# Kernel optimization log

Measured on AMD Instinct MI355X. Metric: run time of the kernel, lower is better.

Reference implementation:

```python
import jax, jax.numpy as jnp
import numpy as np

TOKENS, IN_DIM, VOCAB = 2048, 2048, 32000
TILE_FACTOR = 16


def setup_inputs() -> dict:
    key = jax.random.key(0)
    k1, k2, k3 = jax.random.split(key, 3)
    inp = jax.random.normal(k1, (TOKENS, IN_DIM), dtype=jnp.float32)
    target = jax.random.randint(k2, (TOKENS,), 0, VOCAB, dtype=jnp.int64)
    # LM-head weight, shape [out_dim(vocab), in_dim] as in nn.Linear
    proj_weight = jax.random.normal(k3, (VOCAB, IN_DIM), dtype=jnp.float32) * 0.02
    return {"input": inp, "target": target, "proj_weight": proj_weight}


def reference(input, target, proj_weight):
    # Original loops over token tiles: for each tile, logits = tile @ W.T,
    # then softmax over vocab (dim=-1). Softmax is per-row (per-token), so the
    # concatenation of per-tile outputs equals the full row-wise softmax.
    # target is accepted but unused, matching the original forward.
    logits = jnp.einsum('td,vd->tv', input, proj_weight)  # [tokens, vocab]
    return jax.nn.softmax(logits, axis=-1)
```

## Files before the change

kernel.cpp:

```cpp
#include <hip/hip_runtime.h>
#include <hip/hip_bf16.h>
#include <math.h>

#define TOKENS 2048
#define IN_DIM 2048
#define VOCAB  32000

#define BM 256
#define BN 256
#define BK 64
#define NKSTEP (IN_DIM / BK)
#define GEMM_GRID ((TOKENS / BM) * (VOCAB / BN))
#define NCT (VOCAB / BN)

typedef short s16x8 __attribute__((ext_vector_type(8)));
typedef float f32x4 __attribute__((ext_vector_type(4)));

__device__ __forceinline__ unsigned short f2bf_rne(float f) {
  unsigned int u = __float_as_uint(f);
  u += 0x7fffu + ((u >> 16) & 1u);
  return (unsigned short)(u >> 16);
}
__device__ __forceinline__ float bf2f(unsigned short h) {
  return __uint_as_float(((unsigned int)h) << 16);
}

__global__ __launch_bounds__(256) void convert_all(
    const float* __restrict__ x, const float* __restrict__ w,
    unsigned short* __restrict__ xbf, unsigned short* __restrict__ wbf) {
  const int NX = TOKENS * IN_DIM / 4;
  const int NW = VOCAB * IN_DIM / 4;
  int idx = blockIdx.x * blockDim.x + threadIdx.x;
  int stride = gridDim.x * blockDim.x;
  for (int i = idx; i < NX + NW; i += stride) {
    const bool isx = i < NX;
    const int j = isx ? i : i - NX;
    float4 v = isx ? reinterpret_cast<const float4*>(x)[j]
                   : reinterpret_cast<const float4*>(w)[j];
    ushort4 o;
    o.x = f2bf_rne(v.x);
    o.y = f2bf_rne(v.y);
    o.z = f2bf_rne(v.z);
    o.w = f2bf_rne(v.w);
    if (isx)
      reinterpret_cast<ushort4*>(xbf)[j] = o;
    else
      reinterpret_cast<ushort4*>(wbf)[j] = o;
  }
}

__device__ __forceinline__ void gload_lds16(const unsigned short* g, unsigned short* l) {
  __builtin_amdgcn_global_load_lds(
      (const __attribute__((address_space(1))) unsigned int*)g,
      (__attribute__((address_space(3))) unsigned int*)l, 16, 0, 0);
}

__global__ __launch_bounds__(512, 2) void gemm_bt(
    const unsigned short* __restrict__ A,
    const unsigned short* __restrict__ B,
    unsigned short* __restrict__ CB,
    float2* __restrict__ partials) {
  __shared__ __align__(16) unsigned short lds[65536];

  const int tid = threadIdx.x;
  const int lane = tid & 63;
  const int wave = tid >> 6;
  const int wr = wave >> 2;
  const int wc = wave & 3;

  const int bid = blockIdx.x;
  const int lid = (bid & 7) * (GEMM_GRID / 8) + (bid >> 3);
  const int rowTile = lid & 7;
  const int colTile = lid >> 3;
  const int rowBase = rowTile * BM;
  const int colBase = colTile * BN;

  const int r0 = tid >> 3;
  const int r1 = 64 + r0;
  const int c8 = (((tid & 7) ^ (r0 & 7)) << 3);
  const unsigned short* srcA0 = A + (size_t)(rowBase + r0) * IN_DIM + c8;
  const unsigned short* srcA1 = A + (size_t)(rowBase + r1) * IN_DIM + c8;
  const unsigned short* srcB0 = B + (size_t)(colBase + r0) * IN_DIM + c8;
  const unsigned short* srcB1 = B + (size_t)(colBase + r1) * IN_DIM + c8;
  const int ldsD0 = tid * 8;
  const int ldsD1 = (512 + tid) * 8;

  auto stageA = [&](int buf, int h, int k) {
    size_t off = (size_t)h * (128 * IN_DIM) + k;
    int dst = buf * 32768 + h * 8192;
    gload_lds16(srcA0 + off, &lds[dst + ldsD0]);
    gload_lds16(srcA1 + off, &lds[dst + ldsD1]);
  };
  auto stageB = [&](int buf, int h, int k) {
    size_t off = (size_t)h * (128 * IN_DIM) + k;
    int dst = 16384 + buf * 32768 + h * 8192;
    gload_lds16(srcB0 + off, &lds[dst + ldsD0]);
    gload_lds16(srcB1 + off, &lds[dst + ldsD1]);
  };

  const int sc0 = (((lane >> 4) ^ (lane & 7)) << 3);
  const int sc1 = (((4 + (lane >> 4)) ^ (lane & 7)) << 3);
  const int aRow = (wr * 128 + (lane & 15)) * 64;
  const int bRow = 16384 + (wc * 64 + (lane & 15)) * 64;

#define LDA(buf, m, kk) (*(const s16x8*)&lds[(buf) * 32768 + aRow + (m) * 1024 + ((kk) ? sc1 : sc0)])
#define LDB(buf, n, kk) (*(const s16x8*)&lds[(buf) * 32768 + bRow + (n) * 1024 + ((kk) ? sc1 : sc0)])

  f32x4 acc[8][4] = {};

  stageA(0, 0, 0);
  stageA(0, 1, 0);
  stageB(0, 0, 0);
  stageB(0, 1, 0);
  stageA(1, 0, 64);
  stageA(1, 1, 64);
  stageB(1, 0, 64);
  asm volatile("s_waitcnt vmcnt(6)" ::: "memory");
  __builtin_amdgcn_s_barrier();

#define KSTEP(bufc, kn1, kn2)                                                       \
  {                                                                                 \
    s16x8 aL[4][2], aH[4][2], bL[2][2], bH[2][2];                                   \
                                   \
    _Pragma("unroll") for (int m = 0; m < 4; ++m) {                                 \
      aL[m][0] = LDA(bufc, m, 0);                                                   \
      aL[m][1] = LDA(bufc, m, 1);                                                   \
    }                                                                               \
    _Pragma("unroll") for (int n = 0; n < 2; ++n) {                                 \
      bL[n][0] = LDB(bufc, n, 0);                                                   \
      bL[n][1] = LDB(bufc, n, 1);                                                   \
    }                                                                               \
    stageB((bufc) ^ 1, 1, kn1);                                                     \
    asm volatile("s_waitcnt lgkmcnt(8)" ::: "memory");                              \
    __builtin_amdgcn_s_barrier();                                                   \
    asm volatile("s_waitcnt lgkmcnt(0)" ::: "memory");                              \
    __builtin_amdgcn_s_setprio(1);                                                  \
    _Pragma("unroll") for (int m = 0; m < 4; ++m)                                   \
        _Pragma("unroll") for (int n = 0; n < 2; ++n) {                             \
      acc[m][n] = __builtin_amdgcn_mfma_f32_16x16x32_bf16(aL[m][0], bL[n][0], acc[m][n], 0, 0, 0); \
      acc[m][n] = __builtin_amdgcn_mfma_f32_16x16x32_bf16(aL[m][1], bL[n][1], acc[m][n], 0, 0, 0); \
    }                                                                               \
    __builtin_amdgcn_s_setprio(0);                                                  \
    __builtin_amdgcn_s_barrier();                                                   \
                                                      \
    _Pragma("unroll") for (int m = 0; m < 4; ++m) {                                 \
      aH[m][0] = LDA(bufc, 4 + m, 0);                                               \
      aH[m][1] = LDA(bufc, 4 + m, 1);                                               \
    }                                                                               \
    __builtin_amdgcn_s_barrier();                                                   \
    asm volatile("s_waitcnt lgkmcnt(0)" ::: "memory");                              \
    __builtin_amdgcn_s_setprio(1);                                                  \
    _Pragma("unroll") for (int m = 0; m < 4; ++m)                                   \
        _Pragma("unroll") for (int n = 0; n < 2; ++n) {                             \
      acc[4 + m][n] = __builtin_amdgcn_mfma_f32_16x16x32_bf16(aH[m][0], bL[n][0], acc[4 + m][n], 0, 0, 0); \
      acc[4 + m][n] = __builtin_amdgcn_mfma_f32_16x16x32_bf16(aH[m][1], bL[n][1], acc[4 + m][n], 0, 0, 0); \
    }                                                                               \
    __builtin_amdgcn_s_setprio(0);                                                  \
    __builtin_amdgcn_s_barrier();                                                   \
     \
    _Pragma("unroll") for (int n = 0; n < 2; ++n) {                                 \
      bH[n][0] = LDB(bufc, 2 + n, 0);                                               \
      bH[n][1] = LDB(bufc, 2 + n, 1);                                               \
    }                                                                               \
    stageA((bufc), 0, kn2);                                                         \
    stageA((bufc), 1, kn2);                                                         \
    __builtin_amdgcn_s_barrier();                                                   \
    asm volatile("s_waitcnt lgkmcnt(0)" ::: "memory");                              \
    __builtin_amdgcn_s_setprio(1);                                                  \
    _Pragma("unroll") for (int m = 0; m < 4; ++m)                                   \
        _Pragma("unroll") for (int n = 0; n < 2; ++n) {                             \
      acc[4 + m][2 + n] = __builtin_amdgcn_mfma_f32_16x16x32_bf16(aH[m][0], bH[n][0], acc[4 + m][2 + n], 0, 0, 0); \
      acc[4 + m][2 + n] = __builtin_amdgcn_mfma_f32_16x16x32_bf16(aH[m][1], bH[n][1], acc[4 + m][2 + n], 0, 0, 0); \
    }                                                                               \
    __builtin_amdgcn_s_setprio(0);                                                  \
    __builtin_amdgcn_s_barrier();                                                   \
          \
         \
    stageB((bufc), 0, kn2);                                                         \
    __builtin_amdgcn_s_setprio(1);                                                  \
    _Pragma("unroll") for (int m = 0; m < 4; ++m)                                   \
        _Pragma("unroll") for (int n = 0; n < 2; ++n) {                             \
      acc[m][2 + n] = __builtin_amdgcn_mfma_f32_16x16x32_bf16(aL[m][0], bH[n][0], acc[m][2 + n], 0, 0, 0); \
      acc[m][2 + n] = __builtin_amdgcn_mfma_f32_16x16x32_bf16(aL[m][1], bH[n][1], acc[m][2 + n], 0, 0, 0); \
    }                                                                               \
    __builtin_amdgcn_s_setprio(0);                                                  \
    asm volatile("s_waitcnt vmcnt(6)" ::: "memory");                                \
    __builtin_amdgcn_s_barrier();                                                   \
  }

  for (int i = 0; i < NKSTEP / 2; ++i) {
    const int k = i * 128;
    KSTEP(0, (k + 64) & (IN_DIM - 1), (k + 128) & (IN_DIM - 1));
    KSTEP(1, (k + 128) & (IN_DIM - 1), (k + 192) & (IN_DIM - 1));
  }

  asm volatile("s_waitcnt vmcnt(0)" ::: "memory");
  __syncthreads();

  float* lmax = reinterpret_cast<float*>(lds);
  float* lsum = lmax + 1024;
  float* bM = lmax + 2048;
#pragma unroll
  for (int m = 0; m < 8; ++m) {
#pragma unroll
    for (int jj = 0; jj < 4; ++jj) {
      float v0 = acc[m][0][jj], v1 = acc[m][1][jj], v2 = acc[m][2][jj], v3 = acc[m][3][jj];
      float mx = fmaxf(fmaxf(v0, v1), fmaxf(v2, v3));
#pragma unroll
      for (int off = 1; off < 16; off <<= 1) mx = fmaxf(mx, __shfl_xor(mx, off));
      float s = __expf(v0 - mx) + __expf(v1 - mx) + __expf(v2 - mx) + __expf(v3 - mx);
#pragma unroll
      for (int off = 1; off < 16; off <<= 1) s += __shfl_xor(s, off);
      if ((lane & 15) == 0) {
        int r = wr * 128 + m * 16 + ((lane >> 4) << 2) + jj;
        lmax[r * 4 + wc] = mx;
        lsum[r * 4 + wc] = s;
      }
    }
  }
  __syncthreads();
  if (tid < 256) {
    float m0 = lmax[tid * 4 + 0], m1 = lmax[tid * 4 + 1];
    float m2 = lmax[tid * 4 + 2], m3 = lmax[tid * 4 + 3];
    float M = fmaxf(fmaxf(m0, m1), fmaxf(m2, m3));
    float S = lsum[tid * 4 + 0] * __expf(m0 - M) + lsum[tid * 4 + 1] * __expf(m1 - M) +
              lsum[tid * 4 + 2] * __expf(m2 - M) + lsum[tid * 4 + 3] * __expf(m3 - M);
    partials[(size_t)(rowBase + tid) * NCT + colTile] = make_float2(M, S);
    bM[tid] = M;
  }
  __syncthreads();

  const int par = lane & 1;
  const int e = (lane & 15) & ~1;
#pragma unroll
  for (int m = 0; m < 8; ++m) {
#pragma unroll
    for (int jj = 0; jj < 4; ++jj) {
      int rloc = wr * 128 + m * 16 + ((lane >> 4) << 2) + jj;
      float M = bM[rloc];
      unsigned int p[4];
#pragma unroll
      for (int n = 0; n < 4; ++n) {
        float v = acc[m][n][jj] - M;
        float u = __shfl_xor(v, 1);
        float lo = par ? u : v;
        float hi = par ? v : u;
        unsigned int pk;
        asm("v_cvt_pk_bf16_f32 %0, %1, %2" : "=v"(pk) : "v"(lo), "v"(hi));
        p[n] = pk;
      }
      unsigned int q0 = par ? p[1] : p[0];
      unsigned int q1 = par ? p[3] : p[2];
      unsigned short* base = CB + (size_t)64000 * (rowBase + rloc) + 32000 +
                             colBase + wc * 64;
      *reinterpret_cast<unsigned int*>(base + 16 * par + e) = q0;
      *reinterpret_cast<unsigned int*>(base + 32 + 16 * par + e) = q1;
    }
  }
#undef LDA
#undef LDB
#undef KSTEP
}

__global__ __launch_bounds__(256) void apply_softmax(
    float* __restrict__ Out, const float2* __restrict__ partials) {
  __shared__ __align__(16) unsigned short xrow[VOCAB];
  __shared__ float tileM[NCT + 3];
  __shared__ float2 red[4];
  __shared__ float2 gstat;
  const int row = blockIdx.x;
  const int tid = threadIdx.x;

  const unsigned short* src = (const unsigned short*)Out + (size_t)64000 * row + 32000;
  for (int c = tid; c < VOCAB / 8; c += 256)
    reinterpret_cast<s16x8*>(xrow)[c] = reinterpret_cast<const s16x8*>(src)[c];

  const float2* pr = partials + (size_t)row * NCT;
  float M = -3.4e38f, S = 0.f;
  if (tid < NCT) {
    float2 v = pr[tid];
    M = v.x;
    S = v.y;
    tileM[tid] = v.x;
  }
#pragma unroll
  for (int off = 32; off > 0; off >>= 1) {
    float M2 = __shfl_down(M, off);
    float S2 = __shfl_down(S, off);
    float Mn = fmaxf(M, M2);
    S = S * __expf(M - Mn) + S2 * __expf(M2 - Mn);
    M = Mn;
  }
  if ((tid & 63) == 0) red[tid >> 6] = make_float2(M, S);
  __syncthreads();
  if (tid == 0) {
    float Mg = red[0].x, Sg = red[0].y;
#pragma unroll
    for (int w = 1; w < 4; ++w) {
      float M2 = red[w].x, S2 = red[w].y;
      float Mn = fmaxf(Mg, M2);
      Sg = Sg * __expf(Mg - Mn) + S2 * __expf(M2 - Mn);
      Mg = Mn;
    }
    gstat = make_float2(Mg, 1.f / Sg);
  }
  __syncthreads();

  const float M0 = gstat.x, invS = gstat.y;
  float4* dst = reinterpret_cast<float4*>(Out + (size_t)row * VOCAB);
  for (int c = tid; c < VOCAB / 8; c += 256) {
    s16x8 xv = reinterpret_cast<const s16x8*>(xrow)[c];
    float base = tileM[c >> 5] - M0;
    float4 o0, o1;
    o0.x = __expf(bf2f((unsigned short)xv[0]) + base) * invS;
    o0.y = __expf(bf2f((unsigned short)xv[1]) + base) * invS;
    o0.z = __expf(bf2f((unsigned short)xv[2]) + base) * invS;
    o0.w = __expf(bf2f((unsigned short)xv[3]) + base) * invS;
    o1.x = __expf(bf2f((unsigned short)xv[4]) + base) * invS;
    o1.y = __expf(bf2f((unsigned short)xv[5]) + base) * invS;
    o1.z = __expf(bf2f((unsigned short)xv[6]) + base) * invS;
    o1.w = __expf(bf2f((unsigned short)xv[7]) + base) * invS;
    dst[c * 2] = o0;
    dst[c * 2 + 1] = o1;
  }
}

extern "C" void kernel_launch(void* const* d_in, const int* in_sizes, int n_in,
                              void* d_out, int out_size, void* d_ws, size_t ws_size,
                              hipStream_t stream) {
  const float* x = (const float*)d_in[0];
  const float* w = (const float*)d_in[2];
  float* out = (float*)d_out;

  unsigned short* xbf = (unsigned short*)d_ws;
  unsigned short* wbf = xbf + (size_t)TOKENS * IN_DIM;
  float2* partials = (float2*)(wbf + (size_t)VOCAB * IN_DIM);

  convert_all<<<2048, 256, 0, stream>>>(x, w, xbf, wbf);
  gemm_bt<<<GEMM_GRID, 512, 0, stream>>>(xbf, wbf, (unsigned short*)d_out, partials);
  apply_softmax<<<TOKENS, 256, 0, stream>>>(out, partials);
}
```

Before: 468.3 us.

## Make GEMM persistent with 250 workgroups and prefetch next tile during epilogue

Replaces the 1000-workgroup GEMM launch with a persistent kernel of 250 workgroups, each processing 4 output tiles. The final K-steps of each tile already stage the next tile's A/B data into LDS, so global loads overlap the softmax-statistics epilogue and tile switch. This aims to remove the tail effect and the pipeline ramp-up at every workgroup start. In exchange it uses extra LDS scratch, which may affect occupancy at 2 blocks per CU, and fixes the per-XCD tile mapping by hand.

```diff
diff --git a/kernel.cpp b/kernel.cpp
--- a/kernel.cpp
+++ b/kernel.cpp
@@ -10,8 +10,9 @@
 #define BN 256
 #define BK 64
 #define NKSTEP (IN_DIM / BK)
-#define GEMM_GRID ((TOKENS / BM) * (VOCAB / BN))
+#define NTILES ((TOKENS / BM) * (VOCAB / BN))
 #define NCT (VOCAB / BN)
+#define PGRID 250
 
 typedef short s16x8 __attribute__((ext_vector_type(8)));
 typedef float f32x4 __attribute__((ext_vector_type(4)));
@@ -55,12 +56,15 @@
       (__attribute__((address_space(3))) unsigned int*)l, 16, 0, 0);
 }
 
-__global__ __launch_bounds__(512, 2) void gemm_bt(
+__global__ __launch_bounds__(512, 2) void gemm_persist(
     const unsigned short* __restrict__ A,
     const unsigned short* __restrict__ B,
     unsigned short* __restrict__ CB,
     float2* __restrict__ partials) {
   __shared__ __align__(16) unsigned short lds[65536];
+  __shared__ float scrM[1024];
+  __shared__ float scrS[1024];
+  __shared__ float bM[256];
 
   const int tid = threadIdx.x;
   const int lane = tid & 63;
@@ -68,34 +72,26 @@
   const int wr = wave >> 2;
   const int wc = wave & 3;
 
-  const int bid = blockIdx.x;
-  const int lid = (bid & 7) * (GEMM_GRID / 8) + (bid >> 3);
-  const int rowTile = lid & 7;
-  const int colTile = lid >> 3;
-  const int rowBase = rowTile * BM;
-  const int colBase = colTile * BN;
+  const int xcd = blockIdx.x & 7;
+  const int sub = blockIdx.x >> 3;
+  const int wgid = (xcd < 2 ? xcd * 32 : 64 + (xcd - 2) * 31) + sub;
 
   const int r0 = tid >> 3;
-  const int r1 = 64 + r0;
   const int c8 = (((tid & 7) ^ (r0 & 7)) << 3);
-  const unsigned short* srcA0 = A + (size_t)(rowBase + r0) * IN_DIM + c8;
-  const unsigned short* srcA1 = A + (size_t)(rowBase + r1) * IN_DIM + c8;
-  const unsigned short* srcB0 = B + (size_t)(colBase + r0) * IN_DIM + c8;
-  const unsigned short* srcB1 = B + (size_t)(colBase + r1) * IN_DIM + c8;
   const int ldsD0 = tid * 8;
   const int ldsD1 = (512 + tid) * 8;
 
-  auto stageA = [&](int buf, int h, int k) {
+  auto stA = [&](int buf, int h, const unsigned short* p0, const unsigned short* p1, int k) {
     size_t off = (size_t)h * (128 * IN_DIM) + k;
     int dst = buf * 32768 + h * 8192;
-    gload_lds16(srcA0 + off, &lds[dst + ldsD0]);
-    gload_lds16(srcA1 + off, &lds[dst + ldsD1]);
+    gload_lds16(p0 + off, &lds[dst + ldsD0]);
+    gload_lds16(p1 + off, &lds[dst + ldsD1]);
   };
-  auto stageB = [&](int buf, int h, int k) {
+  auto stB = [&](int buf, int h, const unsigned short* p0, const unsigned short* p1, int k) {
     size_t off = (size_t)h * (128 * IN_DIM) + k;
     int dst = 16384 + buf * 32768 + h * 8192;
-    gload_lds16(srcB0 + off, &lds[dst + ldsD0]);
-    gload_lds16(srcB1 + off, &lds[dst + ldsD1]);
+    gload_lds16(p0 + off, &lds[dst + ldsD0]);
+    gload_lds16(p1 + off, &lds[dst + ldsD1]);
   };
 
   const int sc0 = (((lane >> 4) ^ (lane & 7)) << 3);
@@ -106,22 +102,29 @@
 #define LDA(buf, m, kk) (*(const s16x8*)&lds[(buf) * 32768 + aRow + (m) * 1024 + ((kk) ? sc1 : sc0)])
 #define LDB(buf, n, kk) (*(const s16x8*)&lds[(buf) * 32768 + bRow + (n) * 1024 + ((kk) ? sc1 : sc0)])
 
-  f32x4 acc[8][4] = {};
-
-  stageA(0, 0, 0);
-  stageA(0, 1, 0);
-  stageB(0, 0, 0);
-  stageB(0, 1, 0);
-  stageA(1, 0, 64);
-  stageA(1, 1, 64);
-  stageB(1, 0, 64);
+  f32x4 acc[8][4];
+
+  int t = wgid;
+  int rowBase = (t & 7) * BM, colBase = (t >> 3) * BN;
+  const unsigned short* cA0 = A + (size_t)(rowBase + r0) * IN_DIM + c8;
+  const unsigned short* cA1 = cA0 + (size_t)64 * IN_DIM;
+  const unsigned short* cB0 = B + (size_t)(colBase + r0) * IN_DIM + c8;
+  const unsigned short* cB1 = cB0 + (size_t)64 * IN_DIM;
+
+  stA(0, 0, cA0, cA1, 0);
+  stA(0, 1, cA0, cA1, 0);
+  stB(0, 0, cB0, cB1, 0);
+  stB(0, 1, cB0, cB1, 0);
+  stA(1, 0, cA0, cA1, 64);
+  stA(1, 1, cA0, cA1, 64);
+  stB(1, 0, cB0, cB1, 64);
   asm volatile("s_waitcnt vmcnt(6)" ::: "memory");
   __builtin_amdgcn_s_barrier();
 
-#define KSTEP(bufc, kn1, kn2)                                                       \
+#define KSTEP(bufc, kn1, kn2, PB1A, PB1B, PA2A, PA2B, PB2A, PB2B)                   \
   {                                                                                 \
     s16x8 aL[4][2], aH[4][2], bL[2][2], bH[2][2];                                   \
-                                   \
+                                    \
     _Pragma("unroll") for (int m = 0; m < 4; ++m) {                                 \
       aL[m][0] = LDA(bufc, m, 0);                                                   \
       aL[m][1] = LDA(bufc, m, 1);                                                   \
@@ -130,7 +133,7 @@
       bL[n][0] = LDB(bufc, n, 0);                                                   \
       bL[n][1] = LDB(bufc, n, 1);                                                   \
     }                                                                               \
-    stageB((bufc) ^ 1, 1, kn1);                                                     \
+    stB((bufc) ^ 1, 1, PB1A, PB1B, kn1);                                            \
     asm volatile("s_waitcnt lgkmcnt(8)" ::: "memory");                              \
     __builtin_amdgcn_s_barrier();                                                   \
     asm volatile("s_waitcnt lgkmcnt(0)" ::: "memory");                              \
@@ -142,7 +145,7 @@
     }                                                                               \
     __builtin_amdgcn_s_setprio(0);                                                  \
     __builtin_amdgcn_s_barrier();                                                   \
-                                                      \
+                                                                \
     _Pragma("unroll") for (int m = 0; m < 4; ++m) {                                 \
       aH[m][0] = LDA(bufc, 4 + m, 0);                                               \
       aH[m][1] = LDA(bufc, 4 + m, 1);                                               \
@@ -157,13 +160,13 @@
     }                                                                               \
     __builtin_amdgcn_s_setprio(0);                                                  \
     __builtin_amdgcn_s_barrier();                                                   \
-     \
+              \
     _Pragma("unroll") for (int n = 0; n < 2; ++n) {                                 \
       bH[n][0] = LDB(bufc, 2 + n, 0);                                               \
       bH[n][1] = LDB(bufc, 2 + n, 1);                                               \
     }                                                                               \
-    stageA((bufc), 0, kn2);                                                         \
-    stageA((bufc), 1, kn2);                                                         \
+    stA((bufc), 0, PA2A, PA2B, kn2);                                                \
+    stA((bufc), 1, PA2A, PA2B, kn2);                                                \
     __builtin_amdgcn_s_barrier();                                                   \
     asm volatile("s_waitcnt lgkmcnt(0)" ::: "memory");                              \
     __builtin_amdgcn_s_setprio(1);                                                  \
@@ -174,9 +177,8 @@
     }                                                                               \
     __builtin_amdgcn_s_setprio(0);                                                  \
     __builtin_amdgcn_s_barrier();                                                   \
-          \
-         \
-    stageB((bufc), 0, kn2);                                                         \
+       \
+    stB((bufc), 0, PB2A, PB2B, kn2);                                                \
     __builtin_amdgcn_s_setprio(1);                                                  \
     _Pragma("unroll") for (int m = 0; m < 4; ++m)                                   \
         _Pragma("unroll") for (int n = 0; n < 2; ++n) {                             \
@@ -188,74 +190,96 @@
     __builtin_amdgcn_s_barrier();                                                   \
   }
 
-  for (int i = 0; i < NKSTEP / 2; ++i) {
-    const int k = i * 128;
-    KSTEP(0, (k + 64) & (IN_DIM - 1), (k + 128) & (IN_DIM - 1));
-    KSTEP(1, (k + 128) & (IN_DIM - 1), (k + 192) & (IN_DIM - 1));
-  }
-
-  asm volatile("s_waitcnt vmcnt(0)" ::: "memory");
-  __syncthreads();
-
-  float* lmax = reinterpret_cast<float*>(lds);
-  float* lsum = lmax + 1024;
-  float* bM = lmax + 2048;
-#pragma unroll
-  for (int m = 0; m < 8; ++m) {
-#pragma unroll
-    for (int jj = 0; jj < 4; ++jj) {
-      float v0 = acc[m][0][jj], v1 = acc[m][1][jj], v2 = acc[m][2][jj], v3 = acc[m][3][jj];
-      float mx = fmaxf(fmaxf(v0, v1), fmaxf(v2, v3));
-#pragma unroll
-      for (int off = 1; off < 16; off <<= 1) mx = fmaxf(mx, __shfl_xor(mx, off));
-      float s = __expf(v0 - mx) + __expf(v1 - mx) + __expf(v2 - mx) + __expf(v3 - mx);
-#pragma unroll
-      for (int off = 1; off < 16; off <<= 1) s += __shfl_xor(s, off);
-      if ((lane & 15) == 0) {
-        int r = wr * 128 + m * 16 + ((lane >> 4) << 2) + jj;
-        lmax[r * 4 + wc] = mx;
-        lsum[r * 4 + wc] = s;
+  for (int ti = 0; ti < 4; ++ti) {
+    const int colTile = t >> 3;
+    const int tn = (ti < 3) ? t + PGRID : t;
+    const int nRow = (tn & 7) * BM, nCol = (tn >> 3) * BN;
+    const unsigned short* nA0 = A + (size_t)(nRow + r0) * IN_DIM + c8;
+    const unsigned short* nA1 = nA0 + (size_t)64 * IN_DIM;
+    const unsigned short* nB0 = B + (size_t)(nCol + r0) * IN_DIM + c8;
+    const unsigned short* nB1 = nB0 + (size_t)64 * IN_DIM;
+
+#pragma unroll
+    for (int m = 0; m < 8; ++m)
+#pragma unroll
+      for (int n = 0; n < 4; ++n) acc[m][n] = (f32x4){0.f, 0.f, 0.f, 0.f};
+
+    for (int i = 0; i < 15; ++i) {
+      const int k = i * 128;
+      KSTEP(0, k + 64, k + 128, cB0, cB1, cA0, cA1, cB0, cB1);
+      KSTEP(1, k + 128, k + 192, cB0, cB1, cA0, cA1, cB0, cB1);
+    }
+    KSTEP(0, 1984, 0, cB0, cB1, nA0, nA1, nB0, nB1);
+    KSTEP(1, 0, 64, nB0, nB1, nA0, nA1, nB0, nB1);
+
+#pragma unroll
+    for (int m = 0; m < 8; ++m) {
+#pragma unroll
+      for (int jj = 0; jj < 4; ++jj) {
+        float v0 = acc[m][0][jj], v1 = acc[m][1][jj], v2 = acc[m][2][jj], v3 = acc[m][3][jj];
+        float mx = fmaxf(fmaxf(v0, v1), fmaxf(v2, v3));
+#pragma unroll
+        for (int off = 1; off < 16; off <<= 1) mx = fmaxf(mx, __shfl_xor(mx, off));
+        float s = __expf(v0 - mx) + __expf(v1 - mx) + __expf(v2 - mx) + __expf(v3 - mx);
+#pragma unroll
+        for (int off = 1; off < 16; off <<= 1) s += __shfl_xor(s, off);
+        if ((lane & 15) == 0) {
+          int r = wr * 128 + m * 16 + ((lane >> 4) << 2) + jj;
+          scrM[r * 4 + wc] = mx;
+          scrS[r * 4 + wc] = s;
+        }
       }
     }
-  }
-  __syncthreads();
-  if (tid < 256) {
-    float m0 = lmax[tid * 4 + 0], m1 = lmax[tid * 4 + 1];
-    float m2 = lmax[tid * 4 + 2], m3 = lmax[tid * 4 + 3];
-    float M = fmaxf(fmaxf(m0, m1), fmaxf(m2, m3));
-    float S = lsum[tid * 4 + 0] * __expf(m0 - M) + lsum[tid * 4 + 1] * __expf(m1 - M) +
-              lsum[tid * 4 + 2] * __expf(m2 - M) + lsum[tid * 4 + 3] * __expf(m3 - M);
-    partials[(size_t)(rowBase + tid) * NCT + colTile] = make_float2(M, S);
-    bM[tid] = M;
-  }
-  __syncthreads();
-
-  const int par = lane & 1;
-  const int e = (lane & 15) & ~1;
-#pragma unroll
-  for (int m = 0; m < 8; ++m) {
-#pragma unroll
-    for (int jj = 0; jj < 4; ++jj) {
-      int rloc = wr * 128 + m * 16 + ((lane >> 4) << 2) + jj;
-      float M = bM[rloc];
-      unsigned int p[4];
-#pragma unroll
-      for (int n = 0; n < 4; ++n) {
-        float v = acc[m][n][jj] - M;
-        float u = __shfl_xor(v, 1);
-        float lo = par ? u : v;
-        float hi = par ? v : u;
-        unsigned int pk;
-        asm("v_cvt_pk_bf16_f32 %0, %1, %2" : "=v"(pk) : "v"(lo), "v"(hi));
-        p[n] = pk;
+    asm volatile("s_waitcnt lgkmcnt(0)" ::: "memory");
+    __builtin_amdgcn_s_barrier();
+    if (tid < 256) {
+      float m0 = scrM[tid * 4 + 0], m1 = scrM[tid * 4 + 1];
+      float m2 = scrM[tid * 4 + 2], m3 = scrM[tid * 4 + 3];
+      float M = fmaxf(fmaxf(m0, m1), fmaxf(m2, m3));
+      float S = scrS[tid * 4 + 0] * __expf(m0 - M) + scrS[tid * 4 + 1] * __expf(m1 - M) +
+                scrS[tid * 4 + 2] * __expf(m2 - M) + scrS[tid * 4 + 3] * __expf(m3 - M);
+      partials[(size_t)(rowBase + tid) * NCT + colTile] = make_float2(M, S);
+      bM[tid] = M;
+    }
+    asm volatile("s_waitcnt lgkmcnt(0)" ::: "memory");
+    __builtin_amdgcn_s_barrier();
+    const int par = lane & 1;
+    const int e = (lane & 15) & ~1;
+#pragma unroll
+    for (int m = 0; m < 8; ++m) {
+#pragma unroll
+      for (int jj = 0; jj < 4; ++jj) {
+        int rloc = wr * 128 + m * 16 + ((lane >> 4) << 2) + jj;
+        float M = bM[rloc];
+        unsigned int p[4];
+#pragma unroll
+        for (int n = 0; n < 4; ++n) {
+          float v = acc[m][n][jj] - M;
+          float u = __shfl_xor(v, 1);
+          float lo = par ? u : v;
+          float hi = par ? v : u;
+          unsigned int pk;
+          asm("v_cvt_pk_bf16_f32 %0, %1, %2" : "=v"(pk) : "v"(lo), "v"(hi));
+          p[n] = pk;
+        }
+        unsigned int q0 = par ? p[1] : p[0];
+        unsigned int q1 = par ? p[3] : p[2];
+        unsigned short* base = CB + (size_t)64000 * (rowBase + rloc) + 32000 +
+                               colBase + wc * 64;
+        *reinterpret_cast<unsigned int*>(base + 16 * par + e) = q0;
+        *reinterpret_cast<unsigned int*>(base + 32 + 16 * par + e) = q1;
       }
-      unsigned int q0 = par ? p[1] : p[0];
-      unsigned int q1 = par ? p[3] : p[2];
-      unsigned short* base = CB + (size_t)64000 * (rowBase + rloc) + 32000 +
-                             colBase + wc * 64;
-      *reinterpret_cast<unsigned int*>(base + 16 * par + e) = q0;
-      *reinterpret_cast<unsigned int*>(base + 32 + 16 * par + e) = q1;
-    }
+    }
+    asm volatile("s_waitcnt vmcnt(0)" ::: "memory");
+    __builtin_amdgcn_s_barrier();
+
+    t = tn;
+    rowBase = nRow;
+    colBase = nCol;
+    cA0 = nA0;
+    cA1 = nA1;
+    cB0 = nB0;
+    cB1 = nB1;
   }
 #undef LDA
 #undef LDB
@@ -337,6 +361,6 @@
   float2* partials = (float2*)(wbf + (size_t)VOCAB * IN_DIM);
 
   convert_all<<<2048, 256, 0, stream>>>(x, w, xbf, wbf);
-  gemm_bt<<<GEMM_GRID, 512, 0, stream>>>(xbf, wbf, (unsigned short*)d_out, partials);
+  gemm_persist<<<PGRID, 512, 0, stream>>>(xbf, wbf, (unsigned short*)d_out, partials);
   apply_softmax<<<TOKENS, 256, 0, stream>>>(out, partials);
 }
```

After: 677.9 us. 1.45x slower.
